# Kernel tuning notes

Hardware: AMD Instinct MI355X
Metric: run time of the kernel (lower is better)

The kernel has to match this reference:

```python
import jax, jax.numpy as jnp
import numpy as np

K = 4  # number of neighbors, per kNN-VC convention

def setup_inputs() -> dict:
    key = jax.random.key(0)
    k1, k2 = jax.random.split(key)
    source_feats = jax.random.normal(k1, (2048, 1024), dtype=jnp.float32)
    target_feats = jax.random.normal(k2, (50000, 1024), dtype=jnp.float32)
    return {"source_feats": source_feats, "target_feats": target_feats}

def reference(source_feats, target_feats):
    # cosine kNN matching: for each source frame, find K nearest target frames
    # under cosine distance (= highest cosine similarity), then average them.
    eps = jnp.asarray(1e-8, source_feats.dtype)
    src_n = source_feats / jnp.maximum(jnp.linalg.norm(source_feats, axis=-1, keepdims=True), eps)
    tgt_n = target_feats / jnp.maximum(jnp.linalg.norm(target_feats, axis=-1, keepdims=True), eps)
    # [T_src, T_tgt] cosine similarity
    sims = jnp.einsum('sd,td->st', src_n, tgt_n)
    _, idx = jax.lax.top_k(sims, K)          # [T_src, K]
    neighbors = target_feats[idx]             # [T_src, K, D]
    out = jnp.mean(neighbors, axis=1)         # [T_src, D]
    return out
```

## Files before the change

kernel.cpp:

```cpp
#include <hip/hip_runtime.h>
#include <math.h>

#define S_ROWS 2048
#define T_ROWS 50000
#define DIM    1024
#define KNN    4

#define BM 128
#define BN 128
#define KSL 64
#define NSLAB (DIM / KSL)
#define NBUF 3
#define TILES_PER_CHUNK 2
#define CHUNK_COLS (BN * TILES_PER_CHUNK)
#define NUM_CHUNKS ((T_ROWS + CHUNK_COLS - 1) / CHUNK_COLS)
#define T_PAD (NUM_CHUNKS * CHUNK_COLS)
#define NCAND (NUM_CHUNKS * KNN)
#define REFINE 16
#define SP 67
#define QSCALE 500.0f

typedef unsigned int uint;
typedef unsigned long long u64;
typedef signed char i8;
typedef __attribute__((ext_vector_type(4))) int i32x4;

__device__ __forceinline__ u64 packI(int v, int idx) {
  return ((u64)((uint)v ^ 0x80000000u) << 32) | (uint)(~idx);
}

template <int N>
__device__ __forceinline__ void insU(u64 p, u64 (&tv)[N]) {
  if (p <= tv[N - 1]) return;
  tv[N - 1] = p;
#pragma unroll
  for (int j = N - 1; j > 0; --j) {
    if (tv[j] > tv[j - 1]) { u64 t = tv[j]; tv[j] = tv[j - 1]; tv[j - 1] = t; }
  }
}

__device__ __forceinline__ void llds16(const void* g, void* l) {
  __builtin_amdgcn_global_load_lds(
      reinterpret_cast<__attribute__((address_space(1))) void*>(
          reinterpret_cast<uintptr_t>(g)),
      reinterpret_cast<__attribute__((address_space(3))) void*>(
          (unsigned)reinterpret_cast<uintptr_t>(l)),
      16, 0, 0);
}

__device__ __forceinline__ int imax2(int a, int b) { return a > b ? a : b; }

__global__ __launch_bounds__(256) void quant2_kernel(const float* __restrict__ srcf,
                                                     const float* __restrict__ tgtf,
                                                     i8* __restrict__ srcq,
                                                     i8* __restrict__ tgtq) {
  const int b = blockIdx.x;
  const int tid = threadIdx.x;
  const bool isT = b < T_PAD;
  const int row = isT ? b : b - T_PAD;
  const float* in = isT ? tgtf : srcf;
  i8* outq = isT ? tgtq : srcq;
  const int nvalid = isT ? T_ROWS : S_ROWS;
  if (row >= nvalid) {
    ((uint*)(outq + ((size_t)row << 10)))[tid] = 0u;
    return;
  }
  __shared__ float red[4];
  float4 v = ((const float4*)(in + ((size_t)row << 10)))[tid];
  float s = v.x * v.x + v.y * v.y + v.z * v.z + v.w * v.w;
#pragma unroll
  for (int off = 32; off; off >>= 1) s += __shfl_down(s, off, 64);
  if ((tid & 63) == 0) red[tid >> 6] = s;
  __syncthreads();
  float tot = red[0] + red[1] + red[2] + red[3];
  float r = QSCALE / fmaxf(sqrtf(tot), 1e-8f);
  int q0 = __float2int_rn(v.x * r), q1 = __float2int_rn(v.y * r);
  int q2 = __float2int_rn(v.z * r), q3 = __float2int_rn(v.w * r);
  q0 = imax2(-127, (q0 < 127 ? q0 : 127));
  q1 = imax2(-127, (q1 < 127 ? q1 : 127));
  q2 = imax2(-127, (q2 < 127 ? q2 : 127));
  q3 = imax2(-127, (q3 < 127 ? q3 : 127));
  uint packed = ((uint)q0 & 255u) | (((uint)q1 & 255u) << 8) |
                (((uint)q2 & 255u) << 16) | (((uint)q3 & 255u) << 24);
  ((uint*)(outq + ((size_t)row << 10)))[tid] = packed;
}

union __align__(16) SimSmem {
  i8 ab[NBUF][2 * BM * KSL];
  int sims[BM * SP];
  u64 mb[256 * KNN];
};

__device__ __forceinline__ void stage64(const i8* aP, const i8* bP, i8* aL, i8* bL) {
  llds16(aP, aL);
  llds16(aP + 16384, aL + 1024);
  llds16(bP, bL);
  llds16(bP + 16384, bL + 1024);
}

__global__ __launch_bounds__(256) void sim_i8_kernel(const i8* __restrict__ srcq,
                                                     const i8* __restrict__ tgtq,
                                                     u64* __restrict__ partials) {
  __shared__ SimSmem sm;

  const int tid = threadIdx.x;
  const int lane = tid & 63;
  const int wave = tid >> 6;
  const int qr = (wave >> 1) * 64;
  const int qch = wave & 1;
  const int m = lane & 15;
  const int quad = lane >> 4;
  const int r0 = blockIdx.x * BM;
  const int chunk = blockIdx.y;

  const int srow4 = lane >> 2;
  const int scb4 = (lane & 3) ^ (srow4 & 3);
  const i8* aLane = srcq + (((size_t)(r0 + wave * 32 + srow4)) << 10) + scb4 * 16;

  const int swz = (quad ^ (m & 3)) << 4;
  const int aoff0 = ((qr + m) << 6) + swz;
  const int boff0 = ((qch * 64 + m) << 6) + swz;

  u64 topp[KNN] = {0, 0, 0, 0};
  int thrI = (int)0x80000000;

  for (int tile = 0; tile < TILES_PER_CHUNK; ++tile) {
    const int c0 = chunk * CHUNK_COLS + tile * BN;
    const i8* bLane = tgtq + (((size_t)(c0 + wave * 32 + srow4)) << 10) + scb4 * 16;

    i32x4 acc[4][4];
#pragma unroll
    for (int i = 0; i < 4; ++i)
#pragma unroll
      for (int j = 0; j < 4; ++j) acc[i][j] = (i32x4){0, 0, 0, 0};

    stage64(aLane, bLane, sm.ab[0] + wave * 2048, sm.ab[0] + 8192 + wave * 2048);
    stage64(aLane + 64, bLane + 64, sm.ab[1] + wave * 2048, sm.ab[1] + 8192 + wave * 2048);

#pragma unroll
    for (int k = 0; k < NSLAB; ++k) {
      if (k == NSLAB - 1)
        asm volatile("s_waitcnt vmcnt(0)" ::: "memory");
      else
        asm volatile("s_waitcnt vmcnt(4)" ::: "memory");
      asm volatile("s_waitcnt lgkmcnt(0)" ::: "memory");
      __builtin_amdgcn_s_barrier();
      __builtin_amdgcn_sched_barrier(0);

      const i8* base = sm.ab[k % NBUF];
      i32x4 af[4], bf[4];
#pragma unroll
      for (int i = 0; i < 4; ++i) af[i] = *(const i32x4*)(base + aoff0 + i * 1024);
#pragma unroll
      for (int j = 0; j < 4; ++j) bf[j] = *(const i32x4*)(base + 8192 + boff0 + j * 1024);

      if (k + 2 < NSLAB) {
        i8* nb = sm.ab[(k + 2) % NBUF];
        stage64(aLane + ((k + 2) << 6), bLane + ((k + 2) << 6),
                nb + wave * 2048, nb + 8192 + wave * 2048);
      }

      __builtin_amdgcn_s_setprio(1);
#pragma unroll
      for (int i = 0; i < 4; ++i)
#pragma unroll
        for (int j = 0; j < 4; ++j)
          acc[i][j] = __builtin_amdgcn_mfma_i32_16x16x64_i8(af[i], bf[j], acc[i][j], 0, 0, 0);
      __builtin_amdgcn_s_setprio(0);
    }

    __syncthreads();

#pragma unroll
    for (int ph = 0; ph < 2; ++ph) {
      if (qch == ph) {
#pragma unroll
        for (int i = 0; i < 4; ++i)
#pragma unroll
          for (int j = 0; j < 4; ++j)
#pragma unroll
            for (int reg = 0; reg < 4; ++reg)
              sm.sims[(qr + i * 16 + quad * 4 + reg) * SP + j * 16 + m] = acc[i][j][reg];
      }
      __syncthreads();
      {
        const int rowl = tid & 127;
        const int chh = tid >> 7;
        const int* srow = &sm.sims[rowl * SP + chh * 32];
        const int gbase = c0 + ph * 64 + chh * 32;
#pragma unroll
        for (int c = 0; c < 32; c += 4) {
          int a = srow[c], b = srow[c + 1], d2 = srow[c + 2], e = srow[c + 3];
          int mx = imax2(imax2(a, b), imax2(d2, e));
          if (mx > thrI) {
            const int g = gbase + c;
            if (g + 0 < T_ROWS) insU<KNN>(packI(a, g + 0), topp);
            if (g + 1 < T_ROWS) insU<KNN>(packI(b, g + 1), topp);
            if (g + 2 < T_ROWS) insU<KNN>(packI(d2, g + 2), topp);
            if (g + 3 < T_ROWS) insU<KNN>(packI(e, g + 3), topp);
            thrI = (int)((uint)(topp[KNN - 1] >> 32) ^ 0x80000000u);
          }
        }
      }
      __syncthreads();
    }
  }

#pragma unroll
  for (int j = 0; j < KNN; ++j) sm.mb[tid * KNN + j] = topp[j];
  __syncthreads();
  if (tid < 128) {
#pragma unroll
    for (int j = 0; j < KNN; ++j) insU<KNN>(sm.mb[(tid + 128) * KNN + j], topp);
    u64* dst = partials + ((size_t)(r0 + tid) * NUM_CHUNKS + chunk) * KNN;
#pragma unroll
    for (int j = 0; j < KNN; ++j) dst[j] = topp[j];
  }
}

__global__ __launch_bounds__(256) void merge_gather_kernel(
    const u64* __restrict__ partials, const float* __restrict__ src,
    const float* __restrict__ tgt, float* __restrict__ out) {
  const int row = blockIdx.x;
  const int tid = threadIdx.x;
  const int lane = tid & 63;
  const int wave = tid >> 6;
  __shared__ u64 cbuf[NCAND];
  __shared__ u64 part8[8][REFINE];
  __shared__ int cand[REFINE];
  __shared__ double cval[REFINE];
  __shared__ int fin[KNN];

  for (int c = tid; c < NCAND; c += 256) cbuf[c] = partials[(size_t)row * NCAND + c];
  __syncthreads();

  if (tid < 8) {
    u64 t16[REFINE];
#pragma unroll
    for (int j = 0; j < REFINE; ++j) t16[j] = 0;
    const int base = tid * (NCAND / 8);
    for (int c = 0; c < NCAND / 8; ++c) insU<REFINE>(cbuf[base + c], t16);
#pragma unroll
    for (int j = 0; j < REFINE; ++j) part8[tid][j] = t16[j];
  }
  __syncthreads();
  if (tid == 0) {
    u64 t16[REFINE];
#pragma unroll
    for (int j = 0; j < REFINE; ++j) t16[j] = 0;
    for (int s = 0; s < 8; ++s)
#pragma unroll
      for (int j = 0; j < REFINE; ++j) insU<REFINE>(part8[s][j], t16);
#pragma unroll
    for (int j = 0; j < REFINE; ++j) cand[j] = (int)(~(uint)t16[j]);
  }
  __syncthreads();

  const float4* s4 = (const float4*)(src + ((size_t)row << 10));
  float4 s0 = s4[lane], s1 = s4[lane + 64], s2 = s4[lane + 128], s3 = s4[lane + 192];
  double ss = (double)s0.x * s0.x + (double)s0.y * s0.y + (double)s0.z * s0.z + (double)s0.w * s0.w
            + (double)s1.x * s1.x + (double)s1.y * s1.y + (double)s1.z * s1.z + (double)s1.w * s1.w
            + (double)s2.x * s2.x + (double)s2.y * s2.y + (double)s2.z * s2.z + (double)s2.w * s2.w
            + (double)s3.x * s3.x + (double)s3.y * s3.y + (double)s3.z * s3.z + (double)s3.w * s3.w;
#pragma unroll
  for (int off = 32; off; off >>= 1) ss += __shfl_down(ss, off, 64);
  ss = __shfl(ss, 0, 64);
  const double sn = fmax(sqrt(ss), 1e-8);

  for (int cc = wave; cc < REFINE; cc += 4) {
    const float4* t4 = (const float4*)(tgt + ((size_t)cand[cc] << 10));
    float4 t0 = t4[lane], t1 = t4[lane + 64], t2 = t4[lane + 128], t3 = t4[lane + 192];
    double dd = (double)s0.x * t0.x + (double)s0.y * t0.y + (double)s0.z * t0.z + (double)s0.w * t0.w
              + (double)s1.x * t1.x + (double)s1.y * t1.y + (double)s1.z * t1.z + (double)s1.w * t1.w
              + (double)s2.x * t2.x + (double)s2.y * t2.y + (double)s2.z * t2.z + (double)s2.w * t2.w
              + (double)s3.x * t3.x + (double)s3.y * t3.y + (double)s3.z * t3.z + (double)s3.w * t3.w;
    double tt = (double)t0.x * t0.x + (double)t0.y * t0.y + (double)t0.z * t0.z + (double)t0.w * t0.w
              + (double)t1.x * t1.x + (double)t1.y * t1.y + (double)t1.z * t1.z + (double)t1.w * t1.w
              + (double)t2.x * t2.x + (double)t2.y * t2.y + (double)t2.z * t2.z + (double)t2.w * t2.w
              + (double)t3.x * t3.x + (double)t3.y * t3.y + (double)t3.z * t3.z + (double)t3.w * t3.w;
#pragma unroll
    for (int off = 32; off; off >>= 1) {
      dd += __shfl_down(dd, off, 64);
      tt += __shfl_down(tt, off, 64);
    }
    if (lane == 0) cval[cc] = dd / (sn * fmax(sqrt(tt), 1e-8));
  }
  __syncthreads();

  if (tid == 0) {
    bool used[REFINE];
#pragma unroll
    for (int j = 0; j < REFINE; ++j) used[j] = false;
    for (int k = 0; k < KNN; ++k) {
      int bj = -1; double bv = 0.0; int bidx = 0x7fffffff;
      for (int j = 0; j < REFINE; ++j) {
        if (used[j]) continue;
        if (bj < 0 || cval[j] > bv || (cval[j] == bv && cand[j] < bidx)) {
          bj = j; bv = cval[j]; bidx = cand[j];
        }
      }
      used[bj] = true;
      fin[k] = cand[bj];
    }
  }
  __syncthreads();

  const int d = tid * 4;
  float4 a = *(const float4*)(tgt + ((size_t)fin[0] << 10) + d);
  float4 b = *(const float4*)(tgt + ((size_t)fin[1] << 10) + d);
  float4 c = *(const float4*)(tgt + ((size_t)fin[2] << 10) + d);
  float4 e = *(const float4*)(tgt + ((size_t)fin[3] << 10) + d);
  float4 o;
  o.x = 0.25f * (a.x + b.x + c.x + e.x);
  o.y = 0.25f * (a.y + b.y + c.y + e.y);
  o.z = 0.25f * (a.z + b.z + c.z + e.z);
  o.w = 0.25f * (a.w + b.w + c.w + e.w);
  *(float4*)(out + ((size_t)row << 10) + d) = o;
}

extern "C" void kernel_launch(void* const* d_in, const int* in_sizes, int n_in,
                              void* d_out, int out_size, void* d_ws, size_t ws_size,
                              hipStream_t stream) {
  const float* src = (const float*)d_in[0];
  const float* tgt = (const float*)d_in[1];
  float* out = (float*)d_out;
  char* ws = (char*)d_ws;

  const size_t SRCQ_B = (size_t)S_ROWS << 10;
  const size_t TGTQ_B = (size_t)T_PAD << 10;

  i8* srcq = (i8*)ws;
  i8* tgtq = (i8*)(ws + SRCQ_B);
  u64* partials = (u64*)(ws + SRCQ_B + TGTQ_B);

  quant2_kernel<<<T_PAD + S_ROWS, 256, 0, stream>>>(src, tgt, srcq, tgtq);

  dim3 g3(S_ROWS / BM, NUM_CHUNKS);
  sim_i8_kernel<<<g3, 256, 0, stream>>>(srcq, tgtq, partials);

  merge_gather_kernel<<<S_ROWS, 256, 0, stream>>>(partials, src, tgt, out);
}
```

Baseline: 666.6 us.

## Widen similarity tile to 128x256 per block with double-buffered LDS slabs

Measured after the change: 808.5 us. +21.3%, slower.

```diff
diff --git a/kernel.cpp b/kernel.cpp
--- a/kernel.cpp
+++ b/kernel.cpp
@@ -7,12 +7,11 @@
 #define KNN    4
 
 #define BM 128
-#define BN 128
+#define BN 256
 #define KSL 64
 #define NSLAB (DIM / KSL)
-#define NBUF 3
-#define TILES_PER_CHUNK 2
-#define CHUNK_COLS (BN * TILES_PER_CHUNK)
+#define NBUF 2
+#define CHUNK_COLS BN
 #define NUM_CHUNKS ((T_ROWS + CHUNK_COLS - 1) / CHUNK_COLS)
 #define T_PAD (NUM_CHUNKS * CHUNK_COLS)
 #define NCAND (NUM_CHUNKS * KNN)
@@ -86,16 +85,21 @@
 }
 
 union __align__(16) SimSmem {
-  i8 ab[NBUF][2 * BM * KSL];
+  i8 ab[NBUF][(BM + BN) * KSL];
   int sims[BM * SP];
   u64 mb[256 * KNN];
 };
 
-__device__ __forceinline__ void stage64(const i8* aP, const i8* bP, i8* aL, i8* bL) {
+__device__ __forceinline__ void stageSlab(const i8* aP, const i8* bP, i8* bufBase,
+                                          int wave) {
+  i8* aL = bufBase + wave * 2048;
   llds16(aP, aL);
   llds16(aP + 16384, aL + 1024);
+  i8* bL = bufBase + BM * KSL + wave * 4096;
   llds16(bP, bL);
   llds16(bP + 16384, bL + 1024);
+  llds16(bP + 32768, bL + 2048);
+  llds16(bP + 49152, bL + 3072);
 }
 
 __global__ __launch_bounds__(256) void sim_i8_kernel(const i8* __restrict__ srcq,
@@ -106,104 +110,95 @@
   const int tid = threadIdx.x;
   const int lane = tid & 63;
   const int wave = tid >> 6;
-  const int qr = (wave >> 1) * 64;
+  const int wr = wave >> 1;
   const int qch = wave & 1;
   const int m = lane & 15;
   const int quad = lane >> 4;
   const int r0 = blockIdx.x * BM;
   const int chunk = blockIdx.y;
+  const int c0 = chunk * CHUNK_COLS;
 
   const int srow4 = lane >> 2;
   const int scb4 = (lane & 3) ^ (srow4 & 3);
   const i8* aLane = srcq + (((size_t)(r0 + wave * 32 + srow4)) << 10) + scb4 * 16;
+  const i8* bLane = tgtq + (((size_t)(c0 + wave * 64 + srow4)) << 10) + scb4 * 16;
 
   const int swz = (quad ^ (m & 3)) << 4;
-  const int aoff0 = ((qr + m) << 6) + swz;
-  const int boff0 = ((qch * 64 + m) << 6) + swz;
+  const int aoff0 = ((wr * 64 + m) << 6) + swz;
+  const int boff0 = BM * KSL + ((qch * 128 + m) << 6) + swz;
 
   u64 topp[KNN] = {0, 0, 0, 0};
   int thrI = (int)0x80000000;
 
-  for (int tile = 0; tile < TILES_PER_CHUNK; ++tile) {
-    const int c0 = chunk * CHUNK_COLS + tile * BN;
-    const i8* bLane = tgtq + (((size_t)(c0 + wave * 32 + srow4)) << 10) + scb4 * 16;
-
-    i32x4 acc[4][4];
+  i32x4 acc[4][8];
+#pragma unroll
+  for (int i = 0; i < 4; ++i)
+#pragma unroll
+    for (int j = 0; j < 8; ++j) acc[i][j] = (i32x4){0, 0, 0, 0};
+
+  stageSlab(aLane, bLane, sm.ab[0], wave);
+
+#pragma unroll
+  for (int k = 0; k < NSLAB; ++k) {
+    asm volatile("s_waitcnt vmcnt(0)" ::: "memory");
+    asm volatile("s_waitcnt lgkmcnt(0)" ::: "memory");
+    __builtin_amdgcn_s_barrier();
+    __builtin_amdgcn_sched_barrier(0);
+
+    if (k + 1 < NSLAB)
+      stageSlab(aLane + ((k + 1) << 6), bLane + ((k + 1) << 6), sm.ab[(k + 1) & 1], wave);
+
+    const i8* base = sm.ab[k & 1];
+    i32x4 af[4], bf[8];
+#pragma unroll
+    for (int i = 0; i < 4; ++i) af[i] = *(const i32x4*)(base + aoff0 + i * 1024);
+#pragma unroll
+    for (int j = 0; j < 8; ++j) bf[j] = *(const i32x4*)(base + boff0 + j * 1024);
+
+    __builtin_amdgcn_s_setprio(1);
 #pragma unroll
     for (int i = 0; i < 4; ++i)
 #pragma unroll
-      for (int j = 0; j < 4; ++j) acc[i][j] = (i32x4){0, 0, 0, 0};
-
-    stage64(aLane, bLane, sm.ab[0] + wave * 2048, sm.ab[0] + 8192 + wave * 2048);
-    stage64(aLane + 64, bLane + 64, sm.ab[1] + wave * 2048, sm.ab[1] + 8192 + wave * 2048);
-
-#pragma unroll
-    for (int k = 0; k < NSLAB; ++k) {
-      if (k == NSLAB - 1)
-        asm volatile("s_waitcnt vmcnt(0)" ::: "memory");
-      else
-        asm volatile("s_waitcnt vmcnt(4)" ::: "memory");
-      asm volatile("s_waitcnt lgkmcnt(0)" ::: "memory");
-      __builtin_amdgcn_s_barrier();
-      __builtin_amdgcn_sched_barrier(0);
-
-      const i8* base = sm.ab[k % NBUF];
-      i32x4 af[4], bf[4];
-#pragma unroll
-      for (int i = 0; i < 4; ++i) af[i] = *(const i32x4*)(base + aoff0 + i * 1024);
-#pragma unroll
-      for (int j = 0; j < 4; ++j) bf[j] = *(const i32x4*)(base + 8192 + boff0 + j * 1024);
-
-      if (k + 2 < NSLAB) {
-        i8* nb = sm.ab[(k + 2) % NBUF];
-        stage64(aLane + ((k + 2) << 6), bLane + ((k + 2) << 6),
-                nb + wave * 2048, nb + 8192 + wave * 2048);
-      }
-
-      __builtin_amdgcn_s_setprio(1);
+      for (int j = 0; j < 8; ++j)
+        acc[i][j] = __builtin_amdgcn_mfma_i32_16x16x64_i8(af[i], bf[j], acc[i][j], 0, 0, 0);
+    __builtin_amdgcn_s_setprio(0);
+  }
+
+  __syncthreads();
+
+#pragma unroll
+  for (int ph = 0; ph < 4; ++ph) {
+    if (qch == (ph >> 1)) {
 #pragma unroll
       for (int i = 0; i < 4; ++i)
 #pragma unroll
-        for (int j = 0; j < 4; ++j)
-          acc[i][j] = __builtin_amdgcn_mfma_i32_16x16x64_i8(af[i], bf[j], acc[i][j], 0, 0, 0);
-      __builtin_amdgcn_s_setprio(0);
+        for (int j2 = 0; j2 < 4; ++j2)
+#pragma unroll
+          for (int reg = 0; reg < 4; ++reg)
+            sm.sims[(wr * 64 + i * 16 + quad * 4 + reg) * SP + j2 * 16 + m] =
+                acc[i][(ph & 1) * 4 + j2][reg];
     }
-
     __syncthreads();
-
-#pragma unroll
-    for (int ph = 0; ph < 2; ++ph) {
-      if (qch == ph) {
-#pragma unroll
-        for (int i = 0; i < 4; ++i)
-#pragma unroll
-          for (int j = 0; j < 4; ++j)
-#pragma unroll
-            for (int reg = 0; reg < 4; ++reg)
-              sm.sims[(qr + i * 16 + quad * 4 + reg) * SP + j * 16 + m] = acc[i][j][reg];
-      }
-      __syncthreads();
-      {
-        const int rowl = tid & 127;
-        const int chh = tid >> 7;
-        const int* srow = &sm.sims[rowl * SP + chh * 32];
-        const int gbase = c0 + ph * 64 + chh * 32;
-#pragma unroll
-        for (int c = 0; c < 32; c += 4) {
-          int a = srow[c], b = srow[c + 1], d2 = srow[c + 2], e = srow[c + 3];
-          int mx = imax2(imax2(a, b), imax2(d2, e));
-          if (mx > thrI) {
-            const int g = gbase + c;
-            if (g + 0 < T_ROWS) insU<KNN>(packI(a, g + 0), topp);
-            if (g + 1 < T_ROWS) insU<KNN>(packI(b, g + 1), topp);
-            if (g + 2 < T_ROWS) insU<KNN>(packI(d2, g + 2), topp);
-            if (g + 3 < T_ROWS) insU<KNN>(packI(e, g + 3), topp);
-            thrI = (int)((uint)(topp[KNN - 1] >> 32) ^ 0x80000000u);
-          }
+    {
+      const int rowl = tid & 127;
+      const int chh = tid >> 7;
+      const int* srow = &sm.sims[rowl * SP + chh * 32];
+      const int gbase = c0 + ph * 64 + chh * 32;
+#pragma unroll
+      for (int c = 0; c < 32; c += 4) {
+        int a = srow[c], b = srow[c + 1], d2 = srow[c + 2], e = srow[c + 3];
+        int mx = imax2(imax2(a, b), imax2(d2, e));
+        if (mx > thrI) {
+          const int g = gbase + c;
+          if (g + 0 < T_ROWS) insU<KNN>(packI(a, g + 0), topp);
+          if (g + 1 < T_ROWS) insU<KNN>(packI(b, g + 1), topp);
+          if (g + 2 < T_ROWS) insU<KNN>(packI(d2, g + 2), topp);
+          if (g + 3 < T_ROWS) insU<KNN>(packI(e, g + 3), topp);
+          thrI = (int)((uint)(topp[KNN - 1] >> 32) ^ 0x80000000u);
         }
       }
-      __syncthreads();
     }
+    __syncthreads();
   }
 
 #pragma unroll
```
